# Performance work log

Measured on AMD Instinct MI355X. Metric: run time of the kernel, lower is better.

Reference implementation:

```python
import math
import jax, jax.numpy as jnp
import numpy as np

EMBED_DIM = 1024
NUM_HEADS = 16
HEAD_DIM = EMBED_DIM // NUM_HEADS


def setup_inputs() -> dict:
    key = jax.random.key(0)
    k1, k2, k3, k4 = jax.random.split(key, 4)
    B, S = 4, 2048
    x = jax.random.normal(k1, (B, S, EMBED_DIM), dtype=jnp.float32)
    mask = jnp.ones((B, S), dtype=jnp.int32)  # key-padding mask, 1 = keep
    # nn.Linear(embed_dim, 3*embed_dim, bias=False): weight [3E, E]
    w_qkv = jax.random.normal(k2, (3 * EMBED_DIM, EMBED_DIM), dtype=jnp.float32) / math.sqrt(EMBED_DIM)
    # nn.Linear(embed_dim, embed_dim): weight [E, E], bias [E]
    w_out = jax.random.normal(k3, (EMBED_DIM, EMBED_DIM), dtype=jnp.float32) / math.sqrt(EMBED_DIM)
    b_out = jax.random.normal(k4, (EMBED_DIM,), dtype=jnp.float32) * 0.01
    return {"x": x, "w_qkv": w_qkv, "w_out": w_out, "b_out": b_out, "mask": mask}


def _attention(x, w_qkv, w_out, b_out, mask):
    B, S, E = x.shape
    qkv = jnp.einsum("bse,fe->bsf", x, w_qkv)  # [B,S,3E]
    q, k, v = jnp.split(qkv, 3, axis=-1)
    def heads(t):  # [B,S,E] -> [B,H,S,D]
        return t.reshape(B, S, NUM_HEADS, HEAD_DIM).transpose(0, 2, 1, 3)
    q, k, v = heads(q), heads(k), heads(v)
    scores = jnp.einsum("bhqd,bhkd->bhqk", q, k) / math.sqrt(HEAD_DIM)
    keep = (mask != 0)[:, None, None, :]  # [B,1,1,S]
    scores = jnp.where(keep, scores, jnp.float32(-1e9))
    probs = jax.nn.softmax(scores, axis=-1)
    # dropout p=0.0 -> identity (eval semantics)
    out = jnp.einsum("bhqk,bhkd->bhqd", probs, v)
    out = out.transpose(0, 2, 1, 3).reshape(B, S, E)
    return jnp.einsum("bse,fe->bsf", out, w_out) + b_out


def reference(x, w_qkv, w_out, b_out, mask):
    return _attention(x, w_qkv, w_out, b_out, mask)
```

## Files before the change

kernel.cpp:

```cpp
#include <hip/hip_runtime.h>

#define EMB 1024
#define NH 16
#define HD 64
#define SEQ 2048
#define BB 4

typedef __attribute__((ext_vector_type(8))) short bf8;
typedef __attribute__((ext_vector_type(4))) short bf4;
typedef __attribute__((ext_vector_type(4))) float f4;

#define MFMA16(a, b, c) __builtin_amdgcn_mfma_f32_16x16x32_bf16((a), (b), (c), 0, 0, 0)

#if defined(__has_builtin)
#if __has_builtin(__builtin_amdgcn_mfma_f32_16x16x16_bf16_1k)
#define HAVE_MFMA16X16 1
#endif
#if __has_builtin(__builtin_amdgcn_exp2f)
#define EXP2F __builtin_amdgcn_exp2f
#endif
#if __has_builtin(__builtin_amdgcn_cvt_pk_bf16_f32)
#define HAVE_PK_BF16 1
#endif
#if __has_builtin(__builtin_amdgcn_perm)
#define HAVE_PERM 1
#endif
#endif
#ifndef EXP2F
#define EXP2F exp2f
#endif

__device__ inline f4 pv_mfma(bf4 a, bf4 b, f4 c) {
#ifdef HAVE_MFMA16X16
  return __builtin_amdgcn_mfma_f32_16x16x16_bf16_1k(a, b, c, 0, 0, 0);
#else
  bf8 av, bv;
  *(bf4*)&av = a;  ((int*)&av)[2] = 0; ((int*)&av)[3] = 0;
  *(bf4*)&bv = b;  ((int*)&bv)[2] = 0; ((int*)&bv)[3] = 0;
  return __builtin_amdgcn_mfma_f32_16x16x32_bf16(av, bv, c, 0, 0, 0);
#endif
}

#define GLL16(g, l)                                                     \
  __builtin_amdgcn_global_load_lds(                                     \
      (__attribute__((address_space(1))) void*)(g),                     \
      (__attribute__((address_space(3))) void*)(l), 16, 0, 0)

__device__ inline unsigned short f2bf(float f) {
  union { float f; unsigned u; } v; v.f = f;
  unsigned u = v.u;
  u += 0x7fffu + ((u >> 16) & 1u);
  return (unsigned short)(u >> 16);
}

__device__ inline unsigned pkbf(float a, float b) {
#ifdef HAVE_PK_BF16
  typedef __attribute__((ext_vector_type(2))) __bf16 bf16x2;
  union { bf16x2 v; unsigned u; } c;
  c.v = __builtin_amdgcn_cvt_pk_bf16_f32(a, b);
  return c.u;
#elif defined(HAVE_PERM)
  union { float f; unsigned u; } ua, ub; ua.f = a; ub.f = b;
  return __builtin_amdgcn_perm(ub.u + 0x8000u, ua.u + 0x8000u, 0x07060302u);
#else
  union { float f; unsigned u; } ua, ub; ua.f = a; ub.f = b;
  return ((ua.u + 0x8000u) >> 16) | ((ub.u + 0x8000u) & 0xFFFF0000u);
#endif
}

__global__ void cvt_f32_bf16(const float* __restrict__ in,
                             unsigned short* __restrict__ out, int n4) {
  int i = blockIdx.x * blockDim.x + threadIdx.x;
  if (i < n4) {
    float4 f = ((const float4*)in)[i];
    ushort4 o;
    o.x = f2bf(f.x); o.y = f2bf(f.y); o.z = f2bf(f.z); o.w = f2bf(f.w);
    ((ushort4*)out)[i] = o;
  }
}

template <bool OUTF32>
__global__ __launch_bounds__(256, 2) void gemm_bt(
    const unsigned short* __restrict__ A, const unsigned short* __restrict__ B,
    void* __restrict__ Cout, const float* __restrict__ bias,
    unsigned short* __restrict__ vtb,
    int M, int N, int K, int ldC, int nsplit) {
  __shared__ unsigned short la[128 * 32];
  __shared__ unsigned short lb[128 * 32];

  const int t = threadIdx.x;
  const int lane = t & 63;
  const int w = t >> 6;
  const int quad = lane >> 4;
  const int lcol = lane & 15;
  const int m0 = blockIdx.y * 128;
  const int n0 = blockIdx.x * 128;
  const int wm = (w & 1) * 64;
  const int wn = (w >> 1) * 64;

  f4 acc[4][4];
#pragma unroll
  for (int i = 0; i < 4; i++)
#pragma unroll
    for (int j = 0; j < 4; j++) acc[i][j] = (f4){0.f, 0.f, 0.f, 0.f};

  const int srow = t >> 2;
  const int scol = (t & 3) * 8;
  const unsigned short* gA = A + (size_t)(m0 + srow) * K + scol;
  const unsigned short* gB = B + (size_t)(n0 + srow) * K + scol;
  unsigned short* lA = la + t * 8;
  unsigned short* lB = lb + t * 8;

  for (int kt = 0; kt < K; kt += 32) {
    __syncthreads();
    GLL16(gA + kt, lA);
    GLL16(gA + kt + (size_t)64 * K, lA + 64 * 32);
    GLL16(gB + kt, lB);
    GLL16(gB + kt + (size_t)64 * K, lB + 64 * 32);
    __syncthreads();

    bf8 af[4], bfr[4];
#pragma unroll
    for (int i = 0; i < 4; i++) {
      af[i]  = *(const bf8*)&la[(wm + i * 16 + lcol) * 32 + quad * 8];
      bfr[i] = *(const bf8*)&lb[(wn + i * 16 + lcol) * 32 + quad * 8];
    }
#pragma unroll
    for (int i = 0; i < 4; i++)
#pragma unroll
      for (int j = 0; j < 4; j++)
        acc[i][j] = MFMA16(af[i], bfr[j], acc[i][j]);
  }

  if (!OUTF32 && n0 >= nsplit) {
#pragma unroll
    for (int i = 0; i < 4; i++) {
#pragma unroll
      for (int j = 0; j < 4; j++) {
        int f = n0 + wn + j * 16 + lcol - nsplit;
        int mg = m0 + wm + i * 16 + quad * 4;
        int bb = mg >> 11, ss = mg & 2047;
        ushort4 pk;
        pk.x = f2bf(acc[i][j][0]); pk.y = f2bf(acc[i][j][1]);
        pk.z = f2bf(acc[i][j][2]); pk.w = f2bf(acc[i][j][3]);
        *(ushort4*)&vtb[((size_t)(bb * 1024 + f)) * 2048 + ss] = pk;
      }
    }
  } else {
#pragma unroll
    for (int i = 0; i < 4; i++) {
#pragma unroll
      for (int j = 0; j < 4; j++) {
#pragma unroll
        for (int r = 0; r < 4; r++) {
          int m = m0 + wm + i * 16 + quad * 4 + r;
          int n = n0 + wn + j * 16 + lcol;
          if (OUTF32) {
            float v = acc[i][j][r] + (bias ? bias[n] : 0.f);
            ((float*)Cout)[(size_t)m * ldC + n] = v;
          } else {
            ((unsigned short*)Cout)[(size_t)m * ldC + n] = f2bf(acc[i][j][r]);
          }
        }
      }
    }
  }
}

#define SCALE_LOG2E 0.1803368801111244f
#define BKEEP (-16.0f / SCALE_LOG2E)
#define BDROP (-1e30f / SCALE_LOG2E)

__global__ __launch_bounds__(512, 4) void attn_kernel(
    const unsigned short* __restrict__ qk, const unsigned short* __restrict__ vtg,
    const int* __restrict__ mask, unsigned short* __restrict__ outb) {
  __shared__ unsigned short kv[2 * 8192];
  __shared__ __align__(16) float bt[2][64];

  const int t = threadIdx.x;
  const int lane = t & 63;
  const int w = t >> 6;
  const int quad = lane >> 4;
  const int lcol = lane & 15;
  const int lx = lcol & 7;
  const int q0 = blockIdx.x * 128;
  const int h = blockIdx.y;
  const int b = blockIdx.z;

  const unsigned short* qbase = qk + (size_t)(b * SEQ) * 2048 + h * HD;
  const unsigned short* kbase = qbase + 1024;
  const unsigned short* vbase = vtg + (size_t)((b * 16 + h) * 64) * SEQ;

  const int qrow = q0 + w * 16 + lcol;
  const bf8 qf0 = *(const bf8*)(qbase + (size_t)qrow * 2048 + quad * 8);
  const bf8 qf1 = *(const bf8*)(qbase + (size_t)qrow * 2048 + 32 + quad * 8);

  f4 o[4];
#pragma unroll
  for (int db = 0; db < 4; db++) o[db] = (f4){0.f, 0.f, 0.f, 0.f};
  float lsum = 0.f;

  const int sr = t >> 3;
  const int sc = ((t & 7) ^ (sr & 7)) * 8;
  const unsigned short* gk = kbase + (size_t)sr * 2048 + sc;
  const unsigned short* gv = vbase + (size_t)sr * SEQ + sc;

  const int NT = SEQ / 64;

  GLL16(gk, kv + t * 8);
  GLL16(gv, kv + 4096 + t * 8);
  if (t < 64) bt[0][t] = mask[b * SEQ + t] ? BKEEP : BDROP;
  int pmv = (t < 64) ? mask[b * SEQ + 64 + t] : 0;

  for (int it = 0; it < NT; ++it) {
    const int cur = (it & 1) * 8192;
    __syncthreads();

    if (it + 1 < NT) {
      const int nxt = ((it + 1) & 1) * 8192;
      const size_t k1 = (size_t)(it + 1) * 64;
      GLL16(gk + k1 * 2048, kv + nxt + t * 8);
      GLL16(gv + k1, kv + nxt + 4096 + t * 8);
      if (t < 64) bt[(it + 1) & 1][t] = pmv ? BKEEP : BDROP;
      int kn = (it + 2 < NT) ? (it + 2) * 64 : 0;
      pmv = (t < 64) ? mask[b * SEQ + kn + t] : 0;
    }

    const unsigned short* kcur = kv + cur;
    const unsigned short* vcur = kv + cur + 4096;
    const float* bcur = bt[it & 1];

    f4 sT[4];
#pragma unroll
    for (int kb = 0; kb < 4; kb++) {
      const unsigned short* krow = kcur + (kb * 16 + lcol) * 64;
      bf8 kf0 = *(const bf8*)&krow[(quad ^ lx) * 8];
      bf8 kf1 = *(const bf8*)&krow[((4 + quad) ^ lx) * 8];
      f4 a = *(const f4*)&bcur[kb * 16 + quad * 4];
      a = MFMA16(kf0, qf0, a);
      a = MFMA16(kf1, qf1, a);
      sT[kb] = a;
    }

    bf4 pfrag[4];
#pragma unroll
    for (int kb = 0; kb < 4; kb++) {
      float p0 = EXP2F(sT[kb][0] * SCALE_LOG2E);
      float p1 = EXP2F(sT[kb][1] * SCALE_LOG2E);
      float p2 = EXP2F(sT[kb][2] * SCALE_LOG2E);
      float p3 = EXP2F(sT[kb][3] * SCALE_LOG2E);
      lsum += (p0 + p1) + (p2 + p3);
      union { unsigned u[2]; bf4 s; } cv;
      cv.u[0] = pkbf(p0, p1);
      cv.u[1] = pkbf(p2, p3);
      pfrag[kb] = cv.s;
    }

#pragma unroll
    for (int db = 0; db < 4; db++) {
      const unsigned short* vrow = vcur + (db * 16 + lcol) * 64;
#pragma unroll
      for (int kb = 0; kb < 4; kb++) {
        bf4 vf = *(const bf4*)&vrow[(((kb << 1) | (quad >> 1)) ^ lx) * 8 +
                                    (quad & 1) * 4];
        o[db] = pv_mfma(vf, pfrag[kb], o[db]);
      }
    }
  }

  lsum += __shfl_xor(lsum, 16);
  lsum += __shfl_xor(lsum, 32);
  float inv = 1.f / lsum;
#pragma unroll
  for (int db = 0; db < 4; db++) {
    ushort4 pk;
    pk.x = f2bf(o[db][0] * inv);
    pk.y = f2bf(o[db][1] * inv);
    pk.z = f2bf(o[db][2] * inv);
    pk.w = f2bf(o[db][3] * inv);
    *(ushort4*)&outb[(size_t)(b * SEQ + q0 + w * 16 + lcol) * EMB + h * HD +
                     db * 16 + quad * 4] = pk;
  }
}

extern "C" void kernel_launch(void* const* d_in, const int* in_sizes, int n_in,
                              void* d_out, int out_size, void* d_ws, size_t ws_size,
                              hipStream_t stream) {
  const float* x     = (const float*)d_in[0];
  const float* w_qkv = (const float*)d_in[1];
  const float* w_out = (const float*)d_in[2];
  const float* b_out = (const float*)d_in[3];
  const int*   mask  = (const int*)d_in[4];

  char* ws = (char*)d_ws;
  unsigned short* xb    = (unsigned short*)(ws + 0);
  unsigned short* wqkvb = (unsigned short*)(ws + 16777216);
  unsigned short* woutb = (unsigned short*)(ws + 23068672);
  unsigned short* qkb   = (unsigned short*)(ws + 25165824);
  unsigned short* attnb = (unsigned short*)(ws + 58720256);
  unsigned short* vtb   = (unsigned short*)(ws + 75497472);

  cvt_f32_bf16<<<8192, 256, 0, stream>>>(x, xb, 8388608 / 4);
  cvt_f32_bf16<<<3072, 256, 0, stream>>>(w_qkv, wqkvb, 3145728 / 4);
  cvt_f32_bf16<<<1024, 256, 0, stream>>>(w_out, woutb, 1048576 / 4);

  gemm_bt<false><<<dim3(24, 64), 256, 0, stream>>>(
      xb, wqkvb, (void*)qkb, nullptr, vtb, 8192, 3072, 1024, 2048, 2048);

  attn_kernel<<<dim3(16, 16, 4), 512, 0, stream>>>(qkb, vtb, mask, attnb);

  gemm_bt<true><<<dim3(8, 64), 256, 0, stream>>>(
      attnb, woutb, d_out, b_out, nullptr, 8192, 1024, 1024, 1024, 1 << 30);
}
```

Measured before the change: 321.9 us.

## Merge conversion launches, double attention KV tile, remap blocks, add setprio

The three f32-to-bf16 conversion launches become one kernel that writes into the contiguous workspace. The attention kernel now stages 128 keys per iteration instead of 64, which halves the number of barriers and loop trips at the cost of double the LDS (64 KB). Blocks are remapped so that neighbouring block IDs share a head and batch, which should improve L2 reuse of K and V. s_setprio is wrapped around the MFMA phases to favour matrix issue over the exp work. The larger LDS footprint may lower occupancy.

```diff
diff --git a/kernel.cpp b/kernel.cpp
--- a/kernel.cpp
+++ b/kernel.cpp
@@ -68,15 +68,16 @@
 #endif
 }
 
-__global__ void cvt_f32_bf16(const float* __restrict__ in,
-                             unsigned short* __restrict__ out, int n4) {
+__global__ void cvt_all(const float* __restrict__ x, const float* __restrict__ wq,
+                        const float* __restrict__ wo, unsigned short* __restrict__ out) {
   int i = blockIdx.x * blockDim.x + threadIdx.x;
-  if (i < n4) {
-    float4 f = ((const float4*)in)[i];
-    ushort4 o;
-    o.x = f2bf(f.x); o.y = f2bf(f.y); o.z = f2bf(f.z); o.w = f2bf(f.w);
-    ((ushort4*)out)[i] = o;
-  }
+  float4 f;
+  if (i < 2097152)      f = ((const float4*)x)[i];
+  else if (i < 2883584) f = ((const float4*)wq)[i - 2097152];
+  else                  f = ((const float4*)wo)[i - 2883584];
+  ushort4 o;
+  o.x = f2bf(f.x); o.y = f2bf(f.y); o.z = f2bf(f.z); o.w = f2bf(f.w);
+  ((ushort4*)out)[i] = o;
 }
 
 template <bool OUTF32>
@@ -174,8 +175,8 @@
 __global__ __launch_bounds__(512, 4) void attn_kernel(
     const unsigned short* __restrict__ qk, const unsigned short* __restrict__ vtg,
     const int* __restrict__ mask, unsigned short* __restrict__ outb) {
-  __shared__ unsigned short kv[2 * 8192];
-  __shared__ __align__(16) float bt[2][64];
+  __shared__ unsigned short kv[2 * 16384];
+  __shared__ __align__(16) float bt[2][128];
 
   const int t = threadIdx.x;
   const int lane = t & 63;
@@ -183,9 +184,12 @@
   const int quad = lane >> 4;
   const int lcol = lane & 15;
   const int lx = lcol & 7;
-  const int q0 = blockIdx.x * 128;
-  const int h = blockIdx.y;
-  const int b = blockIdx.z;
+
+  const int id = blockIdx.x + (blockIdx.y << 4) + (blockIdx.z << 8);
+  const int g  = (id & 7) + ((id >> 7) << 3);
+  const int q0 = ((id >> 3) & 15) * 128;
+  const int h = g & 15;
+  const int b = g >> 4;
 
   const unsigned short* qbase = qk + (size_t)(b * SEQ) * 2048 + h * HD;
   const unsigned short* kbase = qbase + 1024;
@@ -203,68 +207,81 @@
   const int sr = t >> 3;
   const int sc = ((t & 7) ^ (sr & 7)) * 8;
   const unsigned short* gk = kbase + (size_t)sr * 2048 + sc;
-  const unsigned short* gv = vbase + (size_t)sr * SEQ + sc;
-
-  const int NT = SEQ / 64;
+  const int vd = t >> 4;
+  const int vc8 = ((t & 15) ^ (vd & 7)) * 8;
+  const unsigned short* gv = vbase + (size_t)vd * SEQ + vc8;
+
+  const int NT = SEQ / 128;
 
   GLL16(gk, kv + t * 8);
-  GLL16(gv, kv + 4096 + t * 8);
-  if (t < 64) bt[0][t] = mask[b * SEQ + t] ? BKEEP : BDROP;
-  int pmv = (t < 64) ? mask[b * SEQ + 64 + t] : 0;
+  GLL16(gk + (size_t)64 * 2048, kv + 4096 + t * 8);
+  GLL16(gv, kv + 8192 + t * 8);
+  GLL16(gv + (size_t)32 * SEQ, kv + 12288 + t * 8);
+  if (t < 128) bt[0][t] = mask[b * SEQ + t] ? BKEEP : BDROP;
+  int pmv = (t < 128) ? mask[b * SEQ + 128 + t] : 0;
 
   for (int it = 0; it < NT; ++it) {
-    const int cur = (it & 1) * 8192;
+    const int cur = (it & 1) * 16384;
     __syncthreads();
 
     if (it + 1 < NT) {
-      const int nxt = ((it + 1) & 1) * 8192;
-      const size_t k1 = (size_t)(it + 1) * 64;
+      const int nxt = ((it + 1) & 1) * 16384;
+      const size_t k1 = (size_t)(it + 1) * 128;
       GLL16(gk + k1 * 2048, kv + nxt + t * 8);
-      GLL16(gv + k1, kv + nxt + 4096 + t * 8);
-      if (t < 64) bt[(it + 1) & 1][t] = pmv ? BKEEP : BDROP;
-      int kn = (it + 2 < NT) ? (it + 2) * 64 : 0;
-      pmv = (t < 64) ? mask[b * SEQ + kn + t] : 0;
+      GLL16(gk + (k1 + 64) * 2048, kv + nxt + 4096 + t * 8);
+      GLL16(gv + k1, kv + nxt + 8192 + t * 8);
+      GLL16(gv + (size_t)32 * SEQ + k1, kv + nxt + 12288 + t * 8);
+      if (t < 128) bt[(it + 1) & 1][t] = pmv ? BKEEP : BDROP;
+      int kn = (it + 2 < NT) ? (it + 2) * 128 : 0;
+      pmv = (t < 128) ? mask[b * SEQ + kn + t] : 0;
     }
 
     const unsigned short* kcur = kv + cur;
-    const unsigned short* vcur = kv + cur + 4096;
+    const unsigned short* vcur = kv + cur + 8192;
     const float* bcur = bt[it & 1];
 
-    f4 sT[4];
-#pragma unroll
-    for (int kb = 0; kb < 4; kb++) {
-      const unsigned short* krow = kcur + (kb * 16 + lcol) * 64;
-      bf8 kf0 = *(const bf8*)&krow[(quad ^ lx) * 8];
-      bf8 kf1 = *(const bf8*)&krow[((4 + quad) ^ lx) * 8];
-      f4 a = *(const f4*)&bcur[kb * 16 + quad * 4];
-      a = MFMA16(kf0, qf0, a);
-      a = MFMA16(kf1, qf1, a);
-      sT[kb] = a;
-    }
-
-    bf4 pfrag[4];
-#pragma unroll
-    for (int kb = 0; kb < 4; kb++) {
-      float p0 = EXP2F(sT[kb][0] * SCALE_LOG2E);
-      float p1 = EXP2F(sT[kb][1] * SCALE_LOG2E);
-      float p2 = EXP2F(sT[kb][2] * SCALE_LOG2E);
-      float p3 = EXP2F(sT[kb][3] * SCALE_LOG2E);
-      lsum += (p0 + p1) + (p2 + p3);
-      union { unsigned u[2]; bf4 s; } cv;
-      cv.u[0] = pkbf(p0, p1);
-      cv.u[1] = pkbf(p2, p3);
-      pfrag[kb] = cv.s;
-    }
-
-#pragma unroll
-    for (int db = 0; db < 4; db++) {
-      const unsigned short* vrow = vcur + (db * 16 + lcol) * 64;
+#pragma unroll
+    for (int hh = 0; hh < 2; hh++) {
+      f4 sT[4];
+      __builtin_amdgcn_s_setprio(1);
 #pragma unroll
       for (int kb = 0; kb < 4; kb++) {
-        bf4 vf = *(const bf4*)&vrow[(((kb << 1) | (quad >> 1)) ^ lx) * 8 +
-                                    (quad & 1) * 4];
-        o[db] = pv_mfma(vf, pfrag[kb], o[db]);
-      }
+        const unsigned short* krow = kcur + (hh * 64 + kb * 16 + lcol) * 64;
+        bf8 kf0 = *(const bf8*)&krow[(quad ^ lx) * 8];
+        bf8 kf1 = *(const bf8*)&krow[((4 + quad) ^ lx) * 8];
+        f4 a = *(const f4*)&bcur[hh * 64 + kb * 16 + quad * 4];
+        a = MFMA16(kf0, qf0, a);
+        a = MFMA16(kf1, qf1, a);
+        sT[kb] = a;
+      }
+      __builtin_amdgcn_s_setprio(0);
+
+      bf4 pfrag[4];
+#pragma unroll
+      for (int kb = 0; kb < 4; kb++) {
+        float p0 = EXP2F(sT[kb][0] * SCALE_LOG2E);
+        float p1 = EXP2F(sT[kb][1] * SCALE_LOG2E);
+        float p2 = EXP2F(sT[kb][2] * SCALE_LOG2E);
+        float p3 = EXP2F(sT[kb][3] * SCALE_LOG2E);
+        lsum += (p0 + p1) + (p2 + p3);
+        union { unsigned u[2]; bf4 s; } cv;
+        cv.u[0] = pkbf(p0, p1);
+        cv.u[1] = pkbf(p2, p3);
+        pfrag[kb] = cv.s;
+      }
+
+      __builtin_amdgcn_s_setprio(1);
+#pragma unroll
+      for (int db = 0; db < 4; db++) {
+        const unsigned short* vrow = vcur + (db * 16 + lcol) * 128;
+#pragma unroll
+        for (int kb = 0; kb < 4; kb++) {
+          int c = ((hh * 4 + kb) << 1) | (quad >> 1);
+          bf4 vf = *(const bf4*)&vrow[(c ^ lx) * 8 + (quad & 1) * 4];
+          o[db] = pv_mfma(vf, pfrag[kb], o[db]);
+        }
+      }
+      __builtin_amdgcn_s_setprio(0);
     }
   }
 
@@ -300,9 +317,7 @@
   unsigned short* attnb = (unsigned short*)(ws + 58720256);
   unsigned short* vtb   = (unsigned short*)(ws + 75497472);
 
-  cvt_f32_bf16<<<8192, 256, 0, stream>>>(x, xb, 8388608 / 4);
-  cvt_f32_bf16<<<3072, 256, 0, stream>>>(w_qkv, wqkvb, 3145728 / 4);
-  cvt_f32_bf16<<<1024, 256, 0, stream>>>(w_out, woutb, 1048576 / 4);
+  cvt_all<<<12288, 256, 0, stream>>>(x, w_qkv, w_out, (unsigned short*)ws);
 
   gemm_bt<false><<<dim3(24, 64), 256, 0, stream>>>(
       xb, wqkvb, (void*)qkb, nullptr, vtb, 8192, 3072, 1024, 2048, 2048);
```

New measurement: 312.5 us. 1.03x faster.
